# Kernel optimization log

Hardware: AMD Instinct MI355X
Metric: run time of the kernel (lower is better)

Reference implementation:

```python
import jax, jax.numpy as jnp
import numpy as np

N = 20000      # nodes
E = 320000     # edges (before self loops)
IN = 128       # in_channels
HID = 64       # hid_channels
H = 4          # in_head
OUT = 16       # out_channels (classes)
SLOPE = 0.2    # GATv2 leaky_relu negative_slope default


def setup_inputs() -> dict:
    key = jax.random.key(0)
    ks = jax.random.split(key, 40)
    d = {}
    d["x"] = jax.random.normal(ks[0], (N, IN), jnp.float32)
    src = jax.random.randint(ks[1], (E,), 0, N)
    dst = jax.random.randint(ks[2], (E,), 0, N)
    d["edge_index"] = jnp.stack([src, dst]).astype(jnp.int32)
    # (in_ch, out_ch_per_head, heads) for the 4 GATv2Conv layers
    dims = [(IN, HID, H), (H * HID, HID, H), (H * HID, HID, H), (H * HID, OUT, 1)]
    ki = 3
    for li, (ic, oc, h) in enumerate(dims, 1):
        sc = 1.0 / np.sqrt(ic)
        d[f"w{li}l"] = jax.random.normal(ks[ki], (h * oc, ic), jnp.float32) * sc; ki += 1
        d[f"b{li}l"] = jnp.zeros((h * oc,), jnp.float32)
        d[f"w{li}r"] = jax.random.normal(ks[ki], (h * oc, ic), jnp.float32) * sc; ki += 1
        d[f"b{li}r"] = jnp.zeros((h * oc,), jnp.float32)
        d[f"a{li}"] = jax.random.normal(ks[ki], (h, oc), jnp.float32) * (1.0 / np.sqrt(oc)); ki += 1
        # output bias: [h*oc] if concat else [oc]; layer 4 is concat=False
        d[f"bo{li}"] = jnp.zeros((h * oc if li < 4 else oc,), jnp.float32)
    return d


def gatv2_layer(x, src, dst, wl, bl, wr, br, att, bias, heads, oc, concat):
    n = x.shape[0]
    xl = (x @ wl.T + bl).reshape(n, heads, oc)   # source transform
    xr = (x @ wr.T + br).reshape(n, heads, oc)   # target transform
    # per-edge GATv2 attention logit: a^T LeakyReLU(x_l[src] + x_r[dst])
    e = jax.nn.leaky_relu(xl[src] + xr[dst], SLOPE)          # [E,H,C]
    logits = jnp.einsum('ehc,hc->eh', e, att)                # [E,H]
    # segment softmax over incoming edges of each dst node
    m = jax.ops.segment_max(logits, dst, num_segments=n)     # [N,H]
    ex = jnp.exp(logits - m[dst])
    den = jax.ops.segment_sum(ex, dst, num_segments=n)
    alpha = ex / den[dst]                                    # [E,H]
    out = jax.ops.segment_sum(alpha[..., None] * xl[src], dst, num_segments=n)  # [N,H,C]
    out = out.reshape(n, heads * oc) if concat else out.mean(axis=1)
    return out + bias


def reference(x, edge_index,
              w1l, b1l, w1r, b1r, a1, bo1,
              w2l, b2l, w2r, b2r, a2, bo2,
              w3l, b3l, w3r, b3r, a3, bo3,
              w4l, b4l, w4r, b4r, a4, bo4):
    n = x.shape[0]
    loop = jnp.arange(n, dtype=edge_index.dtype)
    src = jnp.concatenate([edge_index[0], loop])  # PyG GATv2Conv adds self loops
    dst = jnp.concatenate([edge_index[1], loop])
    h = gatv2_layer(x, src, dst, w1l, b1l, w1r, b1r, a1, bo1, H, HID, True)
    h = jax.nn.relu(h)
    h = gatv2_layer(h, src, dst, w2l, b2l, w2r, b2r, a2, bo2, H, HID, True)
    h = jax.nn.relu(h)
    h = gatv2_layer(h, src, dst, w3l, b3l, w3r, b3r, a3, bo3, H, HID, True)
    h = jax.nn.relu(h)
    h = gatv2_layer(h, src, dst, w4l, b4l, w4r, b4r, a4, bo4, 1, OUT, False)
    return h
```

## Files before the change

### kernel.cpp

```cpp
#include <hip/hip_runtime.h>
#include <hip/hip_bf16.h>
#include <math.h>

#define NNODES 20000
#define NEDGES 320000
#define ETOT   (NEDGES + NNODES)
#define SLOPE  0.2f
#define MAXDEG 96

typedef __attribute__((ext_vector_type(8))) short bf16x8;
typedef __attribute__((ext_vector_type(4))) float f32x4;

__device__ inline unsigned short bfbits(float f) {
    __hip_bfloat16 h = __float2bfloat16(f);
    unsigned short u;
    __builtin_memcpy(&u, &h, 2);
    return u;
}
__device__ inline float bf2f(unsigned short u) {
    __hip_bfloat16 h;
    __builtin_memcpy(&h, &u, 2);
    return __bfloat162float(h);
}

__device__ inline void gload_lds16(const unsigned short* g, unsigned short* s) {
    __builtin_amdgcn_global_load_lds(
        (const __attribute__((address_space(1))) unsigned int*)g,
        (__attribute__((address_space(3))) unsigned int*)s, 16, 0, 0);
}

__global__ void slab_fill(const int* __restrict__ ei, int* __restrict__ fill,
                          int* __restrict__ slab) {
    int idx = blockIdx.x * blockDim.x + threadIdx.x;
    if (idx >= ETOT) return;
    int src, dst;
    if (idx < NEDGES) { src = ei[idx]; dst = ei[NEDGES + idx]; }
    else              { src = idx - NEDGES; dst = src; }
    int pos = atomicAdd(&fill[dst], 1);
    if (pos < MAXDEG) slab[dst * MAXDEG + pos] = src;
}

__global__ void convert_x(const float* __restrict__ x, unsigned short* __restrict__ Ap) {
    int idx = blockIdx.x * 256 + threadIdx.x;
    if (idx >= NNODES * 128) return;
    int m = idx >> 7, k = idx & 127;
    float f = x[idx];
    unsigned short hi = bfbits(f);
    unsigned short lo = bfbits(f - bf2f(hi));
    unsigned short* row = Ap + (size_t)m * 384;
    row[k] = hi; row[128 + k] = lo; row[256 + k] = hi;
}

__global__ void convert_w(const float* __restrict__ w0, const float* __restrict__ w1,
                          unsigned short* __restrict__ Wp, int K, int n0, int ntot) {
    int idx = blockIdx.x * 256 + threadIdx.x;
    if (idx >= ntot * K) return;
    int n = idx / K, k = idx - n * K;
    float f = (n < n0) ? w0[n * K + k] : w1[(n - n0) * K + k];
    unsigned short hi = bfbits(f);
    unsigned short lo = bfbits(f - bf2f(hi));
    unsigned short* row = Wp + (size_t)n * 3 * K;
    row[k] = hi; row[K + k] = hi; row[2 * K + k] = lo;
}

template <int NOUT>
__global__ __launch_bounds__(256) void gemm_mfma(
    const unsigned short* __restrict__ Ap, int KP,
    const unsigned short* __restrict__ Wp,
    const float* __restrict__ bias0, const float* __restrict__ bias1,
    float* __restrict__ O0, float* __restrict__ O1)
{
    __shared__ unsigned short Alds[8 * 512];
    __shared__ unsigned short Wlds[8 * 512];

    int m0, nblk;
    if constexpr (NOUT == 512) {
        const int bid = blockIdx.x;
        const int xcd = bid & 7;
        const int k   = bid >> 3;
        nblk = k & 3;
        const int g = (k >> 2) * 8 + xcd;
        if (g >= (NNODES + 127) / 128) return;
        m0 = g * 128;
    } else {
        nblk = 0;
        m0 = blockIdx.x * 128;
    }
    const int n0 = nblk * 128;

    const int tid = threadIdx.x;
    const int l   = tid & 63;
    const int wid = tid >> 6;
    const int wr  = wid >> 1;
    const int wc  = wid & 1;

    const int srow = l & 15;
    const int skb  = l >> 4;

    int arow0 = m0 + wid * 16 + srow;
    int arow1 = arow0 + 64;
    arow0 = min(arow0, NNODES - 1);
    arow1 = min(arow1, NNODES - 1);
    const unsigned short* ag0 = Ap + (size_t)arow0 * KP + skb * 8;
    const unsigned short* ag1 = Ap + (size_t)arow1 * KP + skb * 8;
    int nrow0 = min(n0 + wid * 16 + srow, NOUT - 1);
    int nrow1 = min(n0 + wid * 16 + srow + 64, NOUT - 1);
    const unsigned short* wg0 = Wp + (size_t)nrow0 * KP + skb * 8;
    const unsigned short* wg1 = Wp + (size_t)nrow1 * KP + skb * 8;

    unsigned short* al0 = &Alds[(0 * 4 + wid) * 512];
    unsigned short* al1 = &Alds[(1 * 4 + wid) * 512];
    unsigned short* wl0 = &Wlds[(0 * 4 + wid) * 512];
    unsigned short* wl1 = &Wlds[(1 * 4 + wid) * 512];

    const unsigned short* ard = &Alds[(wr * 4) * 512 + l * 8];
    const unsigned short* wrd = &Wlds[(wc * 4) * 512 + l * 8];

    f32x4 acc[4][4];
    #pragma unroll
    for (int i = 0; i < 4; i++)
        #pragma unroll
        for (int j = 0; j < 4; j++)
            acc[i][j] = (f32x4){0.f, 0.f, 0.f, 0.f};

    for (int k0 = 0; k0 < KP; k0 += 32) {
        gload_lds16(ag0 + k0, al0);
        gload_lds16(ag1 + k0, al1);
        gload_lds16(wg0 + k0, wl0);
        gload_lds16(wg1 + k0, wl1);
        __syncthreads();

        bf16x8 a0 = *(const bf16x8*)(ard + 0 * 512);
        bf16x8 a1 = *(const bf16x8*)(ard + 1 * 512);
        bf16x8 a2 = *(const bf16x8*)(ard + 2 * 512);
        bf16x8 a3 = *(const bf16x8*)(ard + 3 * 512);
        bf16x8 b0 = *(const bf16x8*)(wrd + 0 * 512);
        bf16x8 b1 = *(const bf16x8*)(wrd + 1 * 512);
        bf16x8 b2 = *(const bf16x8*)(wrd + 2 * 512);
        bf16x8 b3 = *(const bf16x8*)(wrd + 3 * 512);

        acc[0][0] = __builtin_amdgcn_mfma_f32_16x16x32_bf16(a0, b0, acc[0][0], 0, 0, 0);
        acc[0][1] = __builtin_amdgcn_mfma_f32_16x16x32_bf16(a0, b1, acc[0][1], 0, 0, 0);
        acc[0][2] = __builtin_amdgcn_mfma_f32_16x16x32_bf16(a0, b2, acc[0][2], 0, 0, 0);
        acc[0][3] = __builtin_amdgcn_mfma_f32_16x16x32_bf16(a0, b3, acc[0][3], 0, 0, 0);
        acc[1][0] = __builtin_amdgcn_mfma_f32_16x16x32_bf16(a1, b0, acc[1][0], 0, 0, 0);
        acc[1][1] = __builtin_amdgcn_mfma_f32_16x16x32_bf16(a1, b1, acc[1][1], 0, 0, 0);
        acc[1][2] = __builtin_amdgcn_mfma_f32_16x16x32_bf16(a1, b2, acc[1][2], 0, 0, 0);
        acc[1][3] = __builtin_amdgcn_mfma_f32_16x16x32_bf16(a1, b3, acc[1][3], 0, 0, 0);
        acc[2][0] = __builtin_amdgcn_mfma_f32_16x16x32_bf16(a2, b0, acc[2][0], 0, 0, 0);
        acc[2][1] = __builtin_amdgcn_mfma_f32_16x16x32_bf16(a2, b1, acc[2][1], 0, 0, 0);
        acc[2][2] = __builtin_amdgcn_mfma_f32_16x16x32_bf16(a2, b2, acc[2][2], 0, 0, 0);
        acc[2][3] = __builtin_amdgcn_mfma_f32_16x16x32_bf16(a2, b3, acc[2][3], 0, 0, 0);
        acc[3][0] = __builtin_amdgcn_mfma_f32_16x16x32_bf16(a3, b0, acc[3][0], 0, 0, 0);
        acc[3][1] = __builtin_amdgcn_mfma_f32_16x16x32_bf16(a3, b1, acc[3][1], 0, 0, 0);
        acc[3][2] = __builtin_amdgcn_mfma_f32_16x16x32_bf16(a3, b2, acc[3][2], 0, 0, 0);
        acc[3][3] = __builtin_amdgcn_mfma_f32_16x16x32_bf16(a3, b3, acc[3][3], 0, 0, 0);

        __syncthreads();
    }

    if constexpr (NOUT == 512) {
        const bool  left = (nblk < 2);
        float*       O   = left ? O0 : O1;
        const float* bs  = left ? bias0 : bias1;
        const int   cb   = (nblk & 1) * 128;
        #pragma unroll
        for (int mi = 0; mi < 4; mi++) {
            int r0 = m0 + wr * 64 + mi * 16 + (l >> 4) * 4;
            #pragma unroll
            for (int ni = 0; ni < 4; ni++) {
                int c = cb + wc * 64 + ni * 16 + (l & 15);
                float bv = bs[c];
                #pragma unroll
                for (int r = 0; r < 4; r++) {
                    int m = r0 + r;
                    if (m < NNODES) O[(size_t)m * 256 + c] = acc[mi][ni][r] + bv;
                }
            }
        }
    } else {
        #pragma unroll
        for (int mi = 0; mi < 4; mi++) {
            int r0 = m0 + wr * 64 + mi * 16 + (l >> 4) * 4;
            #pragma unroll
            for (int ni = 0; ni < 4; ni++) {
                int c = wc * 64 + ni * 16 + (l & 15);
                if (c >= 32) continue;
                float bv = (c < 16) ? bias0[c] : bias1[c - 16];
                #pragma unroll
                for (int r = 0; r < 4; r++) {
                    int m = r0 + r;
                    if (m < NNODES) O0[(size_t)m * 32 + c] = acc[mi][ni][r] + bv;
                }
            }
        }
    }
}

__device__ inline float edge_score(float4 v, float4 xrv, float4 attv) {
    float tx = v.x + xrv.x; tx = fmaxf(tx, SLOPE * tx);
    float ty = v.y + xrv.y; ty = fmaxf(ty, SLOPE * ty);
    float tz = v.z + xrv.z; tz = fmaxf(tz, SLOPE * tz);
    float tw = v.w + xrv.w; tw = fmaxf(tw, SLOPE * tw);
    float s = attv.x * tx + attv.y * ty + attv.z * tz + attv.w * tw;
    s += __shfl_xor(s, 1, 64);
    s += __shfl_xor(s, 2, 64);
    s += __shfl_xor(s, 4, 64);
    s += __shfl_xor(s, 8, 64);
    return s;
}

__device__ inline void sm_update(float s, float4 v, float& m, float& den, float4& acc) {
    float d = s - m;
    bool  r = d > 8.f;
    float e = __expf(r ? -d : d);
    float sc = r ? e : 1.f;
    float pw = r ? 1.f : e;
    m = r ? s : m;
    den = den * sc + pw;
    acc.x = acc.x * sc + pw * v.x;
    acc.y = acc.y * sc + pw * v.y;
    acc.z = acc.z * sc + pw * v.z;
    acc.w = acc.w * sc + pw * v.w;
}

__device__ inline void sm_merge(float& m0, float& den0, float4& acc0,
                                float m1, float den1, float4 acc1) {
    float nm = fmaxf(m0, m1);
    float sa = __expf(m0 - nm);
    float sb = __expf(m1 - nm);
    den0 = den0 * sa + den1 * sb;
    acc0.x = acc0.x * sa + acc1.x * sb;
    acc0.y = acc0.y * sa + acc1.y * sb;
    acc0.z = acc0.z * sa + acc1.z * sb;
    acc0.w = acc0.w * sa + acc1.w * sb;
    m0 = nm;
}

__global__ __launch_bounds__(128) void gat_attn_node(
    const float* __restrict__ xl, const float* __restrict__ xr,
    const float* __restrict__ att, const float* __restrict__ bo,
    const int* __restrict__ fill, const int* __restrict__ slab,
    unsigned short* __restrict__ outp)
{
    const int lane = threadIdx.x & 63;
    const int node = blockIdx.x * 2 + (threadIdx.x >> 6);
    if (node >= NNODES) return;

    const unsigned laneoff = (unsigned)lane << 4;
    const char*    xlb     = (const char*)xl;

    const float4 attv = *(const float4*)&att[lane * 4];
    const float4 xrv  = *(const float4*)((const char*)xr + ((unsigned)node << 10) + laneoff);
    const float4 bov  = *(const float4*)&bo[lane * 4];

    const int  deg = min(fill[node], MAXDEG);
    const int* sl  = slab + node * MAXDEG;

    float  m0 = -1e30f, m1 = -1e30f, m2 = -1e30f, m3 = -1e30f;
    float  d0 = 0.f, d1 = 0.f, d2 = 0.f, d3 = 0.f;
    float4 a0 = make_float4(0.f, 0.f, 0.f, 0.f);
    float4 a1 = a0, a2 = a0, a3 = a0;

    auto gather = [&](int src) -> float4 {
        return *(const float4*)(xlb + (((unsigned)src << 10) + laneoff));
    };

    auto batch = [&](float4 v0, float4 v1, float4 v2, float4 v3) {
        float s0 = edge_score(v0, xrv, attv);
        float s1 = edge_score(v1, xrv, attv);
        float s2 = edge_score(v2, xrv, attv);
        float s3 = edge_score(v3, xrv, attv);
        bool need = (s0 - m0 > 8.f) | (s1 - m1 > 8.f) | (s2 - m2 > 8.f) | (s3 - m3 > 8.f);
        if (!__any(need)) {
            float p0 = __expf(s0 - m0);
            float p1 = __expf(s1 - m1);
            float p2 = __expf(s2 - m2);
            float p3 = __expf(s3 - m3);
            d0 += p0; d1 += p1; d2 += p2; d3 += p3;
            a0.x += p0 * v0.x; a0.y += p0 * v0.y; a0.z += p0 * v0.z; a0.w += p0 * v0.w;
            a1.x += p1 * v1.x; a1.y += p1 * v1.y; a1.z += p1 * v1.z; a1.w += p1 * v1.w;
            a2.x += p2 * v2.x; a2.y += p2 * v2.y; a2.z += p2 * v2.z; a2.w += p2 * v2.w;
            a3.x += p3 * v3.x; a3.y += p3 * v3.y; a3.z += p3 * v3.z; a3.w += p3 * v3.w;
        } else {
            sm_update(s0, v0, m0, d0, a0);
            sm_update(s1, v1, m1, d1, a1);
            sm_update(s2, v2, m2, d2, a2);
            sm_update(s3, v3, m3, d3, a3);
        }
    };

    float4 v0, v1, v2, v3;
    int p = 0;
    if (deg >= 4) {
        int4 s4 = *(const int4*)sl;
        v0 = gather(s4.x); v1 = gather(s4.y);
        v2 = gather(s4.z); v3 = gather(s4.w);
        p = 4;
    }
    for (; p + 4 <= deg; p += 4) {
        int4 s4 = *(const int4*)&sl[p];
        float4 w0 = gather(s4.x);
        float4 w1 = gather(s4.y);
        float4 w2 = gather(s4.z);
        float4 w3 = gather(s4.w);
        batch(v0, v1, v2, v3);
        v0 = w0; v1 = w1; v2 = w2; v3 = w3;
    }
    if (deg >= 4) batch(v0, v1, v2, v3);
    for (; p < deg; ++p) {
        float4 v = gather(sl[p]);
        float s = edge_score(v, xrv, attv);
        sm_update(s, v, m0, d0, a0);
    }

    sm_merge(m0, d0, a0, m1, d1, a1);
    sm_merge(m2, d2, a2, m3, d3, a3);
    sm_merge(m0, d0, a0, m2, d2, a2);

    float4 o;
    o.x = fmaxf(a0.x / d0 + bov.x, 0.f);
    o.y = fmaxf(a0.y / d0 + bov.y, 0.f);
    o.z = fmaxf(a0.z / d0 + bov.z, 0.f);
    o.w = fmaxf(a0.w / d0 + bov.w, 0.f);

    unsigned short* row = outp + (size_t)node * 768 + lane * 4;
    ushort4 hv, lv;
    hv.x = bfbits(o.x); hv.y = bfbits(o.y); hv.z = bfbits(o.z); hv.w = bfbits(o.w);
    lv.x = bfbits(o.x - bf2f(hv.x));
    lv.y = bfbits(o.y - bf2f(hv.y));
    lv.z = bfbits(o.z - bf2f(hv.z));
    lv.w = bfbits(o.w - bf2f(hv.w));
    *(ushort4*)(row)       = hv;
    *(ushort4*)(row + 256) = lv;
    *(ushort4*)(row + 512) = hv;
}

__global__ __launch_bounds__(128) void gat_attn_final(
    const float* __restrict__ O32,
    const float* __restrict__ att, const float* __restrict__ bo,
    const int* __restrict__ fill, const int* __restrict__ slab,
    float* __restrict__ out)
{
    const int lane = threadIdx.x & 63;
    const int sub  = lane >> 4;
    const int c    = lane & 15;

    const int node = (blockIdx.x * 2 + (threadIdx.x >> 6)) * 4 + sub;
    if (node >= NNODES) return;

    const unsigned coff = (unsigned)c << 2;
    const char*    ob   = (const char*)O32;

    const float attc = att[c];
    const float xrc  = *(const float*)(ob + (((unsigned)node << 7) + 64 + coff));

    const int  deg = min(fill[node], MAXDEG);
    const int* sl  = slab + node * MAXDEG;

    float m0 = -1e30f, m1 = -1e30f, d0 = 0.f, d1 = 0.f, a0 = 0.f, a1 = 0.f;

    int p = 0;
    for (; p + 2 <= deg; p += 2) {
        int srcA = sl[p];
        int srcB = sl[p + 1];
        float vA = *(const float*)(ob + (((unsigned)srcA << 7) + coff));
        float vB = *(const float*)(ob + (((unsigned)srcB << 7) + coff));
        float tA = vA + xrc; tA = fmaxf(tA, SLOPE * tA);
        float tB = vB + xrc; tB = fmaxf(tB, SLOPE * tB);
        float sA = attc * tA;
        float sB = attc * tB;
        sA += __shfl_xor(sA, 1, 64);  sB += __shfl_xor(sB, 1, 64);
        sA += __shfl_xor(sA, 2, 64);  sB += __shfl_xor(sB, 2, 64);
        sA += __shfl_xor(sA, 4, 64);  sB += __shfl_xor(sB, 4, 64);
        sA += __shfl_xor(sA, 8, 64);  sB += __shfl_xor(sB, 8, 64);
        {
            float dd = sA - m0; bool r = dd > 8.f;
            float e = __expf(r ? -dd : dd);
            float sc = r ? e : 1.f, pw = r ? 1.f : e;
            m0 = r ? sA : m0;
            d0 = d0 * sc + pw;
            a0 = a0 * sc + pw * vA;
        }
        {
            float dd = sB - m1; bool r = dd > 8.f;
            float e = __expf(r ? -dd : dd);
            float sc = r ? e : 1.f, pw = r ? 1.f : e;
            m1 = r ? sB : m1;
            d1 = d1 * sc + pw;
            a1 = a1 * sc + pw * vB;
        }
    }
    if (p < deg) {
        int src = sl[p];
        float v = *(const float*)(ob + (((unsigned)src << 7) + coff));
        float t = v + xrc; t = fmaxf(t, SLOPE * t);
        float s = attc * t;
        s += __shfl_xor(s, 1, 64);
        s += __shfl_xor(s, 2, 64);
        s += __shfl_xor(s, 4, 64);
        s += __shfl_xor(s, 8, 64);
        float dd = s - m0; bool r = dd > 8.f;
        float e = __expf(r ? -dd : dd);
        float sc = r ? e : 1.f, pw = r ? 1.f : e;
        m0 = r ? s : m0;
        d0 = d0 * sc + pw;
        a0 = a0 * sc + pw * v;
    }

    float nm = fmaxf(m0, m1);
    float sa = __expf(m0 - nm);
    float sb = __expf(m1 - nm);
    float den = d0 * sa + d1 * sb;
    out[(size_t)node * 16 + c] = (a0 * sa + a1 * sb) / den + bo[c];
}

extern "C" void kernel_launch(void* const* d_in, const int* in_sizes, int n_in,
                              void* d_out, int out_size, void* d_ws, size_t ws_size,
                              hipStream_t stream)
{
    const float* x   = (const float*)d_in[0];
    const int*   ei  = (const int*)d_in[1];
    const float* w1l = (const float*)d_in[2];  const float* b1l = (const float*)d_in[3];
    const float* w1r = (const float*)d_in[4];  const float* b1r = (const float*)d_in[5];
    const float* a1  = (const float*)d_in[6];  const float* bo1 = (const float*)d_in[7];
    const float* w2l = (const float*)d_in[8];  const float* b2l = (const float*)d_in[9];
    const float* w2r = (const float*)d_in[10]; const float* b2r = (const float*)d_in[11];
    const float* a2  = (const float*)d_in[12]; const float* bo2 = (const float*)d_in[13];
    const float* w3l = (const float*)d_in[14]; const float* b3l = (const float*)d_in[15];
    const float* w3r = (const float*)d_in[16]; const float* b3r = (const float*)d_in[17];
    const float* a3  = (const float*)d_in[18]; const float* bo3 = (const float*)d_in[19];
    const float* w4l = (const float*)d_in[20]; const float* b4l = (const float*)d_in[21];
    const float* w4r = (const float*)d_in[22]; const float* b4r = (const float*)d_in[23];
    const float* a4  = (const float*)d_in[24]; const float* bo4 = (const float*)d_in[25];

    char* ws = (char*)d_ws;
    auto carve = [&](size_t bytes) {
        void* p = ws;
        ws += (bytes + 255) & ~(size_t)255;
        return p;
    };
    unsigned short* Ap = (unsigned short*)carve((size_t)NNODES * 768 * sizeof(unsigned short));
    float* xl = (float*)carve((size_t)NNODES * 256 * sizeof(float));
    float* xr = (float*)carve((size_t)NNODES * 256 * sizeof(float));
    float* O32 = xl;
    unsigned short* Wp1 = (unsigned short*)carve((size_t)512 * 384 * sizeof(unsigned short));
    unsigned short* Wp2 = (unsigned short*)carve((size_t)512 * 768 * sizeof(unsigned short));
    unsigned short* Wp3 = (unsigned short*)carve((size_t)512 * 768 * sizeof(unsigned short));
    unsigned short* Wp4 = (unsigned short*)carve((size_t)32 * 768 * sizeof(unsigned short));
    int* fill = (int*)carve((size_t)NNODES * sizeof(int));
    int* slab = (int*)carve((size_t)NNODES * MAXDEG * sizeof(int));

    const int eblocks = (ETOT + 255) / 256;

    convert_x<<<(NNODES * 128 + 255) / 256, 256, 0, stream>>>(x, Ap);
    convert_w<<<(512 * 128 + 255) / 256, 256, 0, stream>>>(w1l, w1r, Wp1, 128, 256, 512);
    convert_w<<<(512 * 256 + 255) / 256, 256, 0, stream>>>(w2l, w2r, Wp2, 256, 256, 512);
    convert_w<<<(512 * 256 + 255) / 256, 256, 0, stream>>>(w3l, w3r, Wp3, 256, 256, 512);
    convert_w<<<(32 * 256 + 255) / 256, 256, 0, stream>>>(w4l, w4r, Wp4, 256, 16, 32);

    hipMemsetAsync(fill, 0, (size_t)NNODES * sizeof(int), stream);
    slab_fill<<<eblocks, 256, 0, stream>>>(ei, fill, slab);

    const int g512 = 640;
    const int ablocks = (NNODES + 1) / 2;

    gemm_mfma<512><<<g512, 256, 0, stream>>>(Ap, 384, Wp1, b1l, b1r, xl, xr);
    gat_attn_node<<<ablocks, 128, 0, stream>>>(xl, xr, a1, bo1, fill, slab, Ap);

    gemm_mfma<512><<<g512, 256, 0, stream>>>(Ap, 768, Wp2, b2l, b2r, xl, xr);
    gat_attn_node<<<ablocks, 128, 0, stream>>>(xl, xr, a2, bo2, fill, slab, Ap);

    gemm_mfma<512><<<g512, 256, 0, stream>>>(Ap, 768, Wp3, b3l, b3r, xl, xr);
    gat_attn_node<<<ablocks, 128, 0, stream>>>(xl, xr, a3, bo3, fill, slab, Ap);

    gemm_mfma<32><<<(NNODES + 127) / 128, 256, 0, stream>>>(Ap, 768, Wp4, b4l, b4r, O32, O32);
    gat_attn_final<<<(NNODES + 7) / 8, 128, 0, stream>>>(O32, a4, bo4, fill, slab, (float*)d_out);
}
```

Baseline: 336.7 us.

## Store bf16 hi/lo split once and double-buffer GEMM LDS staging

Activations and weights were stored as three concatenated bf16 chunks (hi,lo,hi / hi,hi,lo) so a single-pass GEMM could compute the 3-term split product. They are now stored as just hi and lo, and the GEMM loads both halves and issues the three MFMAs per tile itself. This cuts global and LDS traffic for the packed operands by a third and shrinks the attention-kernel writes. The K loop also gains a double-buffered LDS stage that prefetches the next tile while computing the current one, which quadruples LDS use per block and may lower occupancy.

```diff
diff --git a/kernel.cpp b/kernel.cpp
--- a/kernel.cpp
+++ b/kernel.cpp
@@ -47,8 +47,8 @@
     float f = x[idx];
     unsigned short hi = bfbits(f);
     unsigned short lo = bfbits(f - bf2f(hi));
-    unsigned short* row = Ap + (size_t)m * 384;
-    row[k] = hi; row[128 + k] = lo; row[256 + k] = hi;
+    unsigned short* row = Ap + (size_t)m * 256;
+    row[k] = hi; row[128 + k] = lo;
 }
 
 __global__ void convert_w(const float* __restrict__ w0, const float* __restrict__ w1,
@@ -59,19 +59,21 @@
     float f = (n < n0) ? w0[n * K + k] : w1[(n - n0) * K + k];
     unsigned short hi = bfbits(f);
     unsigned short lo = bfbits(f - bf2f(hi));
-    unsigned short* row = Wp + (size_t)n * 3 * K;
-    row[k] = hi; row[K + k] = hi; row[2 * K + k] = lo;
+    unsigned short* row = Wp + (size_t)n * 2 * K;
+    row[k] = hi; row[K + k] = lo;
 }
 
 template <int NOUT>
 __global__ __launch_bounds__(256) void gemm_mfma(
-    const unsigned short* __restrict__ Ap, int KP,
+    const unsigned short* __restrict__ Ap, int KK,
     const unsigned short* __restrict__ Wp,
     const float* __restrict__ bias0, const float* __restrict__ bias1,
     float* __restrict__ O0, float* __restrict__ O1)
 {
-    __shared__ unsigned short Alds[8 * 512];
-    __shared__ unsigned short Wlds[8 * 512];
+    __shared__ unsigned short AH[2 * 4096];
+    __shared__ unsigned short AL[2 * 4096];
+    __shared__ unsigned short BH[2 * 4096];
+    __shared__ unsigned short BL[2 * 4096];
 
     int m0, nblk;
     if constexpr (NOUT == 512) {
@@ -96,25 +98,21 @@
 
     const int srow = l & 15;
     const int skb  = l >> 4;
+    const int W2K  = 2 * KK;
 
     int arow0 = m0 + wid * 16 + srow;
     int arow1 = arow0 + 64;
     arow0 = min(arow0, NNODES - 1);
     arow1 = min(arow1, NNODES - 1);
-    const unsigned short* ag0 = Ap + (size_t)arow0 * KP + skb * 8;
-    const unsigned short* ag1 = Ap + (size_t)arow1 * KP + skb * 8;
+    const unsigned short* ahg0 = Ap + (size_t)arow0 * W2K + skb * 8;
+    const unsigned short* ahg1 = Ap + (size_t)arow1 * W2K + skb * 8;
     int nrow0 = min(n0 + wid * 16 + srow, NOUT - 1);
     int nrow1 = min(n0 + wid * 16 + srow + 64, NOUT - 1);
-    const unsigned short* wg0 = Wp + (size_t)nrow0 * KP + skb * 8;
-    const unsigned short* wg1 = Wp + (size_t)nrow1 * KP + skb * 8;
-
-    unsigned short* al0 = &Alds[(0 * 4 + wid) * 512];
-    unsigned short* al1 = &Alds[(1 * 4 + wid) * 512];
-    unsigned short* wl0 = &Wlds[(0 * 4 + wid) * 512];
-    unsigned short* wl1 = &Wlds[(1 * 4 + wid) * 512];
-
-    const unsigned short* ard = &Alds[(wr * 4) * 512 + l * 8];
-    const unsigned short* wrd = &Wlds[(wc * 4) * 512 + l * 8];
+    const unsigned short* bhg0 = Wp + (size_t)nrow0 * W2K + skb * 8;
+    const unsigned short* bhg1 = Wp + (size_t)nrow1 * W2K + skb * 8;
+
+    const int f0 = (0 * 4 + wid) * 512;
+    const int f1 = (1 * 4 + wid) * 512;
 
     f32x4 acc[4][4];
     #pragma unroll
@@ -123,40 +121,51 @@
         for (int j = 0; j < 4; j++)
             acc[i][j] = (f32x4){0.f, 0.f, 0.f, 0.f};
 
-    for (int k0 = 0; k0 < KP; k0 += 32) {
-        gload_lds16(ag0 + k0, al0);
-        gload_lds16(ag1 + k0, al1);
-        gload_lds16(wg0 + k0, wl0);
-        gload_lds16(wg1 + k0, wl1);
+    const int S = KK >> 5;
+
+    auto STAGE = [&](int buf, int k0) {
+        const int bo = buf * 4096;
+        gload_lds16(ahg0 + k0,      &AH[bo + f0]);
+        gload_lds16(ahg1 + k0,      &AH[bo + f1]);
+        gload_lds16(ahg0 + KK + k0, &AL[bo + f0]);
+        gload_lds16(ahg1 + KK + k0, &AL[bo + f1]);
+        gload_lds16(bhg0 + k0,      &BH[bo + f0]);
+        gload_lds16(bhg1 + k0,      &BH[bo + f1]);
+        gload_lds16(bhg0 + KK + k0, &BL[bo + f0]);
+        gload_lds16(bhg1 + KK + k0, &BL[bo + f1]);
+    };
+
+    const int ra = (wr * 4) * 512 + l * 8;
+    const int rb = (wc * 4) * 512 + l * 8;
+
+    STAGE(0, 0);
+    __syncthreads();
+
+    int cur = 0;
+    for (int s = 0; s < S; ++s) {
+        if (s + 1 < S) STAGE(cur ^ 1, (s + 1) * 32);
+
+        const int bo = cur * 4096;
+        bf16x8 ah[4], al_[4], bh[4], bl[4];
+        #pragma unroll
+        for (int i = 0; i < 4; i++) {
+            ah[i]  = *(const bf16x8*)&AH[bo + ra + i * 512];
+            al_[i] = *(const bf16x8*)&AL[bo + ra + i * 512];
+            bh[i]  = *(const bf16x8*)&BH[bo + rb + i * 512];
+            bl[i]  = *(const bf16x8*)&BL[bo + rb + i * 512];
+        }
+
+        #pragma unroll
+        for (int mi = 0; mi < 4; mi++)
+            #pragma unroll
+            for (int ni = 0; ni < 4; ni++) {
+                acc[mi][ni] = __builtin_amdgcn_mfma_f32_16x16x32_bf16(ah[mi],  bh[ni], acc[mi][ni], 0, 0, 0);
+                acc[mi][ni] = __builtin_amdgcn_mfma_f32_16x16x32_bf16(ah[mi],  bl[ni], acc[mi][ni], 0, 0, 0);
+                acc[mi][ni] = __builtin_amdgcn_mfma_f32_16x16x32_bf16(al_[mi], bh[ni], acc[mi][ni], 0, 0, 0);
+            }
+
         __syncthreads();
-
-        bf16x8 a0 = *(const bf16x8*)(ard + 0 * 512);
-        bf16x8 a1 = *(const bf16x8*)(ard + 1 * 512);
-        bf16x8 a2 = *(const bf16x8*)(ard + 2 * 512);
-        bf16x8 a3 = *(const bf16x8*)(ard + 3 * 512);
-        bf16x8 b0 = *(const bf16x8*)(wrd + 0 * 512);
-        bf16x8 b1 = *(const bf16x8*)(wrd + 1 * 512);
-        bf16x8 b2 = *(const bf16x8*)(wrd + 2 * 512);
-        bf16x8 b3 = *(const bf16x8*)(wrd + 3 * 512);
-
-        acc[0][0] = __builtin_amdgcn_mfma_f32_16x16x32_bf16(a0, b0, acc[0][0], 0, 0, 0);
-        acc[0][1] = __builtin_amdgcn_mfma_f32_16x16x32_bf16(a0, b1, acc[0][1], 0, 0, 0);
-        acc[0][2] = __builtin_amdgcn_mfma_f32_16x16x32_bf16(a0, b2, acc[0][2], 0, 0, 0);
-        acc[0][3] = __builtin_amdgcn_mfma_f32_16x16x32_bf16(a0, b3, acc[0][3], 0, 0, 0);
-        acc[1][0] = __builtin_amdgcn_mfma_f32_16x16x32_bf16(a1, b0, acc[1][0], 0, 0, 0);
-        acc[1][1] = __builtin_amdgcn_mfma_f32_16x16x32_bf16(a1, b1, acc[1][1], 0, 0, 0);
-        acc[1][2] = __builtin_amdgcn_mfma_f32_16x16x32_bf16(a1, b2, acc[1][2], 0, 0, 0);
-        acc[1][3] = __builtin_amdgcn_mfma_f32_16x16x32_bf16(a1, b3, acc[1][3], 0, 0, 0);
-        acc[2][0] = __builtin_amdgcn_mfma_f32_16x16x32_bf16(a2, b0, acc[2][0], 0, 0, 0);
-        acc[2][1] = __builtin_amdgcn_mfma_f32_16x16x32_bf16(a2, b1, acc[2][1], 0, 0, 0);
-        acc[2][2] = __builtin_amdgcn_mfma_f32_16x16x32_bf16(a2, b2, acc[2][2], 0, 0, 0);
-        acc[2][3] = __builtin_amdgcn_mfma_f32_16x16x32_bf16(a2, b3, acc[2][3], 0, 0, 0);
-        acc[3][0] = __builtin_amdgcn_mfma_f32_16x16x32_bf16(a3, b0, acc[3][0], 0, 0, 0);
-        acc[3][1] = __builtin_amdgcn_mfma_f32_16x16x32_bf16(a3, b1, acc[3][1], 0, 0, 0);
-        acc[3][2] = __builtin_amdgcn_mfma_f32_16x16x32_bf16(a3, b2, acc[3][2], 0, 0, 0);
-        acc[3][3] = __builtin_amdgcn_mfma_f32_16x16x32_bf16(a3, b3, acc[3][3], 0, 0, 0);
-
-        __syncthreads();
+        cur ^= 1;
     }
 
     if constexpr (NOUT == 512) {
@@ -324,7 +333,7 @@
     o.z = fmaxf(a0.z / d0 + bov.z, 0.f);
     o.w = fmaxf(a0.w / d0 + bov.w, 0.f);
 
-    unsigned short* row = outp + (size_t)node * 768 + lane * 4;
+    unsigned short* row = outp + (size_t)node * 512 + lane * 4;
     ushort4 hv, lv;
     hv.x = bfbits(o.x); hv.y = bfbits(o.y); hv.z = bfbits(o.z); hv.w = bfbits(o.w);
     lv.x = bfbits(o.x - bf2f(hv.x));
@@ -333,7 +342,6 @@
     lv.w = bfbits(o.w - bf2f(hv.w));
     *(ushort4*)(row)       = hv;
     *(ushort4*)(row + 256) = lv;
-    *(ushort4*)(row + 512) = hv;
 }
 
 __global__ __launch_bounds__(128) void gat_attn_final(
@@ -440,14 +448,14 @@
         ws += (bytes + 255) & ~(size_t)255;
         return p;
     };
-    unsigned short* Ap = (unsigned short*)carve((size_t)NNODES * 768 * sizeof(unsigned short));
+    unsigned short* Ap = (unsigned short*)carve((size_t)NNODES * 512 * sizeof(unsigned short));
     float* xl = (float*)carve((size_t)NNODES * 256 * sizeof(float));
     float* xr = (float*)carve((size_t)NNODES * 256 * sizeof(float));
     float* O32 = xl;
-    unsigned short* Wp1 = (unsigned short*)carve((size_t)512 * 384 * sizeof(unsigned short));
-    unsigned short* Wp2 = (unsigned short*)carve((size_t)512 * 768 * sizeof(unsigned short));
-    unsigned short* Wp3 = (unsigned short*)carve((size_t)512 * 768 * sizeof(unsigned short));
-    unsigned short* Wp4 = (unsigned short*)carve((size_t)32 * 768 * sizeof(unsigned short));
+    unsigned short* Wp1 = (unsigned short*)carve((size_t)512 * 256 * sizeof(unsigned short));
+    unsigned short* Wp2 = (unsigned short*)carve((size_t)512 * 512 * sizeof(unsigned short));
+    unsigned short* Wp3 = (unsigned short*)carve((size_t)512 * 512 * sizeof(unsigned short));
+    unsigned short* Wp4 = (unsigned short*)carve((size_t)32 * 512 * sizeof(unsigned short));
     int* fill = (int*)carve((size_t)NNODES * sizeof(int));
     int* slab = (int*)carve((size_t)NNODES * MAXDEG * sizeof(int));
 
@@ -465,15 +473,15 @@
     const int g512 = 640;
     const int ablocks = (NNODES + 1) / 2;
 
-    gemm_mfma<512><<<g512, 256, 0, stream>>>(Ap, 384, Wp1, b1l, b1r, xl, xr);
+    gemm_mfma<512><<<g512, 256, 0, stream>>>(Ap, 128, Wp1, b1l, b1r, xl, xr);
     gat_attn_node<<<ablocks, 128, 0, stream>>>(xl, xr, a1, bo1, fill, slab, Ap);
 
-    gemm_mfma<512><<<g512, 256, 0, stream>>>(Ap, 768, Wp2, b2l, b2r, xl, xr);
+    gemm_mfma<512><<<g512, 256, 0, stream>>>(Ap, 256, Wp2, b2l, b2r, xl, xr);
     gat_attn_node<<<ablocks, 128, 0, stream>>>(xl, xr, a2, bo2, fill, slab, Ap);
 
-    gemm_mfma<512><<<g512, 256, 0, stream>>>(Ap, 768, Wp3, b3l, b3r, xl, xr);
+    gemm_mfma<512><<<g512, 256, 0, stream>>>(Ap, 256, Wp3, b3l, b3r, xl, xr);
     gat_attn_node<<<ablocks, 128, 0, stream>>>(xl, xr, a3, bo3, fill, slab, Ap);
 
-    gemm_mfma<32><<<(NNODES + 127) / 128, 256, 0, stream>>>(Ap, 768, Wp4, b4l, b4r, O32, O32);
+    gemm_mfma<32><<<(NNODES + 127) / 128, 256, 0, stream>>>(Ap, 256, Wp4, b4l, b4r, O32, O32);
     gat_attn_final<<<(NNODES + 7) / 8, 128, 0, stream>>>(O32, a4, bo4, fill, slab, (float*)d_out);
 }
```

After: 327.2 us. 2.8% less time.
